# Performance work log

Measured on AMD Instinct MI355X. Metric: run time of the kernel, lower is better.

Reference implementation:

```python
import jax, jax.numpy as jnp
import numpy as np

B, S, D = 16, 2048, 2048  # S == D required for m_q + output broadcast in original code


def setup_inputs() -> dict:
    key = jax.random.key(0)
    ks = jax.random.split(key, 8)
    scale = 1.0 / np.sqrt(D)
    return {
        "hidden_list": jax.random.normal(ks[0], (B, S, D), dtype=jnp.float32),
        "m_q": jax.random.normal(ks[1], (D,), dtype=jnp.float32),
        "Wq": jax.random.normal(ks[2], (D, D), dtype=jnp.float32) * scale,
        "bq": jax.random.normal(ks[3], (D,), dtype=jnp.float32) * scale,
        "Wm": jax.random.normal(ks[4], (D, D), dtype=jnp.float32) * scale,
        "bm": jax.random.normal(ks[5], (D,), dtype=jnp.float32) * scale,
        "Wa": jax.random.normal(ks[6], (D, D), dtype=jnp.float32) * scale,
        "ba": jax.random.normal(ks[7], (D,), dtype=jnp.float32) * scale,
    }


def reference(hidden_list, m_q, Wq, bq, Wm, bm, Wa, ba):
    # hidden_list: [B, S, D]; m_q: [D]
    hq = jnp.tanh(jnp.einsum("bsd,ed->bse", hidden_list, Wq) + bq)      # [B,S,D]
    mq = jnp.tanh(Wm @ m_q + bm)                                        # [D]
    Sg = hq * mq                                                        # gated bilinear, [B,S,D]
    alpha = jax.nn.softmax(jnp.einsum("bsd,ed->bse", Sg, Wa) + ba, axis=-1)  # [B,S,D]
    output = jnp.sum(alpha * hidden_list, axis=-1)                      # [B,S]
    m_q_new = m_q + output                                              # broadcast [D]+[B,S] (S==D)
    return output, m_q_new
```

## Files before the change

### kernel.cpp

```cpp
#include <hip/hip_runtime.h>

typedef unsigned short u16;
typedef short bf16x8 __attribute__((ext_vector_type(8)));
typedef u16 u16x8 __attribute__((ext_vector_type(8)));
typedef float f32x4 __attribute__((ext_vector_type(4)));

__device__ __forceinline__ float bf2f(u16 u) {
    union { unsigned u; float f; } c; c.u = ((unsigned)u) << 16; return c.f;
}
__device__ __forceinline__ u16 f2bf(float f) {
    union { float f; unsigned u; } c; c.f = f;
    unsigned r = c.u + 0x7FFFu + ((c.u >> 16) & 1u);
    return (u16)(r >> 16);
}
__device__ __forceinline__ float tanh_fast(float x) {
    float e = __expf(2.0f * x);
    return 1.0f - 2.0f / (e + 1.0f);
}
__device__ __forceinline__ void gll16(const void* g, void* l) {
    __builtin_amdgcn_global_load_lds((const __attribute__((address_space(1))) void*)g,
                                     (__attribute__((address_space(3))) void*)l, 16, 0, 0);
}

#define BAR() __builtin_amdgcn_s_barrier()

__global__ __launch_bounds__(256) void cvt_f32_bf16(const float* __restrict__ src,
                                                    u16* __restrict__ dst, int n8) {
    int i = blockIdx.x * blockDim.x + threadIdx.x;
    int stride = gridDim.x * blockDim.x;
    for (; i < n8; i += stride) {
        const float4* s = (const float4*)(src + (size_t)i * 8);
        float4 a = s[0], b = s[1];
        u16x8 o;
        o[0] = f2bf(a.x); o[1] = f2bf(a.y); o[2] = f2bf(a.z); o[3] = f2bf(a.w);
        o[4] = f2bf(b.x); o[5] = f2bf(b.y); o[6] = f2bf(b.z); o[7] = f2bf(b.w);
        *(u16x8*)(dst + (size_t)i * 8) = o;
    }
}

__global__ __launch_bounds__(256) void mq_kernel(const float* __restrict__ Wm,
                                                 const float* __restrict__ q,
                                                 const float* __restrict__ bm,
                                                 float* __restrict__ mq, int D) {
    int w = threadIdx.x >> 6, l = threadIdx.x & 63;
    int e = blockIdx.x * 4 + w;
    const float* wp = Wm + (size_t)e * D;
    float s = 0.f;
    for (int j = 0; j < D; j += 256) {
        float4 wv = *(const float4*)(wp + j + l * 4);
        float4 qv = *(const float4*)(q + j + l * 4);
        s += wv.x * qv.x + wv.y * qv.y + wv.z * qv.z + wv.w * qv.w;
    }
    #pragma unroll
    for (int o = 32; o >= 1; o >>= 1) s += __shfl_xor(s, o);
    if (l == 0) mq[e] = tanh_fast(s + bm[e]);
}

template <int EPI>
__global__ __launch_bounds__(512, 2) void gemm8(const u16* __restrict__ A,
                                                const u16* __restrict__ B,
                                                const float* __restrict__ bias,
                                                const float* __restrict__ gate,
                                                u16* __restrict__ C,
                                                int M, int N, int K) {
    __shared__ u16 sh[65536];
    char* LDS = (char*)sh;
    const int K2 = K * 2;
    const int KT = K >> 6;

    const int tid = threadIdx.x;
    const int w = tid >> 6, l = tid & 63;
    const int wm = w >> 2, wn = w & 3;

    int orig = blockIdx.x + gridDim.x * blockIdx.y;
    int nwg = gridDim.x * gridDim.y;
    int id = ((nwg & 7) == 0) ? ((orig & 7) * (nwg >> 3) + (orig >> 3)) : orig;
    const int tileN = (id % gridDim.x) * 256;
    const int tileM = (id / gridDim.x) * 256;

    const int r0 = (w * 2) * 8 + (l >> 3);
    const int r1 = (w * 2 + 1) * 8 + (l >> 3);
    const int cc = ((l & 7) ^ (l >> 3)) << 4;
    const char* srcA0 = (const char*)A + (size_t)(tileM + r0) * K2 + cc;
    const char* srcA1 = (const char*)A + (size_t)(tileM + r1) * K2 + cc;
    const char* srcB0 = (const char*)B + (size_t)(tileN + r0) * K2 + cc;
    const char* srcB1 = (const char*)B + (size_t)(tileN + r1) * K2 + cc;
    const int ldc0 = (w * 2) * 1024, ldc1 = (w * 2 + 1) * 1024;

#define STG_A(tk, h) do { size_t go = (size_t)(tk) * 128 + (size_t)(h) * 128 * K2; \
    int sb = ((((tk) & 1) * 2 + (h)) * 16384); \
    gll16(srcA0 + go, LDS + sb + ldc0); gll16(srcA1 + go, LDS + sb + ldc1); } while (0)
#define STG_B(tk, h) do { size_t go = (size_t)(tk) * 128 + (size_t)(h) * 128 * K2; \
    int sb = 65536 + ((((tk) & 1) * 2 + (h)) * 16384); \
    gll16(srcB0 + go, LDS + sb + ldc0); gll16(srcB1 + go, LDS + sb + ldc1); } while (0)

    const int sw = l & 7;
    const int rowA = (wm * 64 + (l & 15)) * 128;
    const int rowB = (wn * 32 + (l & 15)) * 128;
    const int ck0 = (((l >> 4) ^ sw) << 4);
    const int ck1 = (((4 + (l >> 4)) ^ sw) << 4);
    const char* pA0 = LDS + rowA + ck0;
    const char* pA1 = LDS + rowA + ck1;
    const char* pB0 = LDS + 65536 + rowB + ck0;
    const char* pB1 = LDS + 65536 + rowB + ck1;

    f32x4 acc[2][4][2][2] = {};

    STG_A(0, 0); STG_B(0, 0); STG_A(0, 1); STG_B(0, 1);
    STG_A(1, 0); STG_B(1, 0);
    asm volatile("s_waitcnt vmcnt(4)" ::: "memory");
    BAR();

#define MFMA_CLUSTER(QM, QN, AF, BF)                                            \
    __builtin_amdgcn_s_setprio(1);                                              \
    _Pragma("unroll")                                                           \
    for (int fm = 0; fm < 4; ++fm)                                              \
        _Pragma("unroll")                                                       \
        for (int fn = 0; fn < 2; ++fn) {                                        \
            acc[QM][fm][QN][fn] = __builtin_amdgcn_mfma_f32_16x16x32_bf16(      \
                AF[fm][0], BF[fn][0], acc[QM][fm][QN][fn], 0, 0, 0);            \
            acc[QM][fm][QN][fn] = __builtin_amdgcn_mfma_f32_16x16x32_bf16(      \
                AF[fm][1], BF[fn][1], acc[QM][fm][QN][fn], 0, 0, 0);            \
        }                                                                       \
    __builtin_amdgcn_s_setprio(0);

#define ITER(t, P) do {                                                         \
    constexpr int A0O = (2 * (P)) * 16384;                                      \
    constexpr int A1O = (2 * (P) + 1) * 16384;                                  \
    bf16x8 af[4][2], b0[2][2], b1[2][2];                                        \
                                   \
    _Pragma("unroll")                                                           \
    for (int fm = 0; fm < 4; ++fm) {                                            \
        af[fm][0] = *(const bf16x8*)(pA0 + A0O + fm * 2048);                    \
        af[fm][1] = *(const bf16x8*)(pA1 + A0O + fm * 2048);                    \
    }                                                                           \
    _Pragma("unroll")                                                           \
    for (int fn = 0; fn < 2; ++fn) {                                            \
        b0[fn][0] = *(const bf16x8*)(pB0 + A0O + fn * 2048);                    \
        b0[fn][1] = *(const bf16x8*)(pB1 + A0O + fn * 2048);                    \
    }                                                                           \
    if ((t) + 1 < KT) STG_A((t) + 1, 1);                                        \
    BAR();                                                                      \
    MFMA_CLUSTER(0, 0, af, b0)                                                  \
    BAR();                                                                      \
                                       \
    _Pragma("unroll")                                                           \
    for (int fn = 0; fn < 2; ++fn) {                                            \
        b1[fn][0] = *(const bf16x8*)(pB0 + A1O + fn * 2048);                    \
        b1[fn][1] = *(const bf16x8*)(pB1 + A1O + fn * 2048);                    \
    }                                                                           \
    if ((t) + 1 < KT) STG_B((t) + 1, 1);                                        \
    BAR();                                                                      \
    MFMA_CLUSTER(0, 1, af, b1)                                                  \
    BAR();                                                                      \
                                       \
    _Pragma("unroll")                                                           \
    for (int fm = 0; fm < 4; ++fm) {                                            \
        af[fm][0] = *(const bf16x8*)(pA0 + A1O + fm * 2048);                    \
        af[fm][1] = *(const bf16x8*)(pA1 + A1O + fm * 2048);                    \
    }                                                                           \
    if ((t) + 2 < KT) STG_A((t) + 2, 0);                                        \
    BAR();                                                                      \
    MFMA_CLUSTER(1, 0, af, b0)                                                  \
    BAR();                                                                      \
                                     \
    if ((t) + 2 < KT) STG_B((t) + 2, 0);                                        \
    BAR();                                                                      \
    MFMA_CLUSTER(1, 1, af, b1)                                                  \
    if ((t) + 2 < KT) asm volatile("s_waitcnt vmcnt(4)" ::: "memory");          \
    else              asm volatile("s_waitcnt vmcnt(0)" ::: "memory");          \
    BAR();                                                                      \
} while (0)

    for (int tt = 0; tt < KT; tt += 2) {
        ITER(tt, 0);
        ITER(tt + 1, 1);
    }
#undef ITER
#undef MFMA_CLUSTER
#undef STG_A
#undef STG_B

    const int cr = (l >> 4) * 4;
    const int cl = l & 15;
    #pragma unroll
    for (int qn = 0; qn < 2; ++qn)
        #pragma unroll
        for (int fn = 0; fn < 2; ++fn) {
            const int col = tileN + qn * 128 + wn * 32 + fn * 16 + cl;
            const float bs = bias[col];
            float gt = 0.f;
            if (EPI == 0) gt = gate[col];
            #pragma unroll
            for (int qm = 0; qm < 2; ++qm)
                #pragma unroll
                for (int fm = 0; fm < 4; ++fm)
                    #pragma unroll
                    for (int r = 0; r < 4; ++r) {
                        const int row = tileM + qm * 128 + wm * 64 + fm * 16 + cr + r;
                        float v = acc[qm][fm][qn][fn][r] + bs;
                        if (EPI == 0) v = tanh_fast(v) * gt;
                        C[(size_t)row * N + col] = f2bf(v);
                    }
        }
}

__global__ __launch_bounds__(256) void softmax_out(const u16* __restrict__ logits,
                                                   const float* __restrict__ hidden,
                                                   const float* __restrict__ m_q,
                                                   float* __restrict__ out,
                                                   int D, int R) {
    const int r = blockIdx.x;
    const int t = threadIdx.x;
    const int w = t >> 6, l = t & 63;
    const u16* lp = logits + (size_t)r * D + t * 8;
    const float* hp = hidden + (size_t)r * D + t * 8;

    bf16x8 lv = *(const bf16x8*)lp;
    float lf[8];
    #pragma unroll
    for (int j = 0; j < 8; ++j) lf[j] = bf2f((u16)lv[j]);
    float4 h0 = *(const float4*)hp;
    float4 h1 = *(const float4*)(hp + 4);
    float hv[8] = {h0.x, h0.y, h0.z, h0.w, h1.x, h1.y, h1.z, h1.w};

    float m = lf[0];
    #pragma unroll
    for (int j = 1; j < 8; ++j) m = fmaxf(m, lf[j]);
    #pragma unroll
    for (int o = 32; o >= 1; o >>= 1) m = fmaxf(m, __shfl_xor(m, o));

    __shared__ float red[8];
    if (l == 0) red[w] = m;
    __syncthreads();
    m = fmaxf(fmaxf(red[0], red[1]), fmaxf(red[2], red[3]));
    __syncthreads();

    float se = 0.f, sh = 0.f;
    #pragma unroll
    for (int j = 0; j < 8; ++j) {
        float e = __expf(lf[j] - m);
        se += e;
        sh += e * hv[j];
    }
    #pragma unroll
    for (int o = 32; o >= 1; o >>= 1) { se += __shfl_xor(se, o); sh += __shfl_xor(sh, o); }
    if (l == 0) { red[w] = se; red[4 + w] = sh; }
    __syncthreads();
    if (t == 0) {
        float SE = red[0] + red[1] + red[2] + red[3];
        float SH = red[4] + red[5] + red[6] + red[7];
        float o = SH / SE;
        out[r] = o;
        out[R + r] = m_q[r & (D - 1)] + o;
    }
}

extern "C" void kernel_launch(void* const* d_in, const int* in_sizes, int n_in,
                              void* d_out, int out_size, void* d_ws, size_t ws_size,
                              hipStream_t stream) {
    const float* hidden = (const float*)d_in[0];
    const float* m_q    = (const float*)d_in[1];
    const float* Wq     = (const float*)d_in[2];
    const float* bq     = (const float*)d_in[3];
    const float* Wm     = (const float*)d_in[4];
    const float* bm     = (const float*)d_in[5];
    const float* Wa     = (const float*)d_in[6];
    const float* ba     = (const float*)d_in[7];
    float* out = (float*)d_out;

    const int D = 2048;
    const int M = 16 * 2048;

    char* ws = (char*)d_ws;
    size_t oH  = 0;
    size_t oS  = oH  + (size_t)M * D * 2;
    size_t oWq = oS  + (size_t)M * D * 2;
    size_t oWa = oWq + (size_t)D * D * 2;
    size_t oMq = oWa + (size_t)D * D * 2;
    size_t need = oMq + (size_t)D * sizeof(float);
    if (ws_size < need) return;

    u16* hbf    = (u16*)(ws + oH);
    u16* Sg     = (u16*)(ws + oS);
    u16* Wqb    = (u16*)(ws + oWq);
    u16* Wab    = (u16*)(ws + oWa);
    float* mq   = (float*)(ws + oMq);
    u16* logits = hbf;

    cvt_f32_bf16<<<4096, 256, 0, stream>>>(hidden, hbf, M * D / 8);
    cvt_f32_bf16<<<1024, 256, 0, stream>>>(Wq, Wqb, D * D / 8);
    cvt_f32_bf16<<<1024, 256, 0, stream>>>(Wa, Wab, D * D / 8);
    mq_kernel<<<D / 4, 256, 0, stream>>>(Wm, m_q, bm, mq, D);

    dim3 grid(D / 256, M / 256);
    gemm8<0><<<grid, 512, 0, stream>>>(hbf, Wqb, bq, mq, Sg, M, D, D);
    gemm8<1><<<grid, 512, 0, stream>>>(Sg, Wab, ba, nullptr, logits, M, D, D);

    softmax_out<<<M, 256, 0, stream>>>(logits, hidden, m_q, out, D, M);
}
```

Measured before the change: 660.4 us.

## Fuse second GEMM with online softmax and weighted row reduction

Replaces the second GEMM plus the separate softmax kernel with one kernel. Each block owns 128 rows and loops over all 8 column tiles of Wa, keeping a running max, denominator and numerator per row, so the bf16 logits matrix is never written or read back. The weighting now uses the bf16 copy of hidden instead of the fp32 original, and the block walks N sequentially, giving a 256-block grid with smaller tiles. It also adds several barriers per column tile for the cross-wave reductions.

```diff
diff --git a/kernel.cpp b/kernel.cpp
--- a/kernel.cpp
+++ b/kernel.cpp
@@ -56,7 +56,6 @@
     if (l == 0) mq[e] = tanh_fast(s + bm[e]);
 }
 
-template <int EPI>
 __global__ __launch_bounds__(512, 2) void gemm8(const u16* __restrict__ A,
                                                 const u16* __restrict__ B,
                                                 const float* __restrict__ bias,
@@ -128,7 +127,6 @@
     constexpr int A0O = (2 * (P)) * 16384;                                      \
     constexpr int A1O = (2 * (P) + 1) * 16384;                                  \
     bf16x8 af[4][2], b0[2][2], b1[2][2];                                        \
-                                   \
     _Pragma("unroll")                                                           \
     for (int fm = 0; fm < 4; ++fm) {                                            \
         af[fm][0] = *(const bf16x8*)(pA0 + A0O + fm * 2048);                    \
@@ -143,7 +141,6 @@
     BAR();                                                                      \
     MFMA_CLUSTER(0, 0, af, b0)                                                  \
     BAR();                                                                      \
-                                       \
     _Pragma("unroll")                                                           \
     for (int fn = 0; fn < 2; ++fn) {                                            \
         b1[fn][0] = *(const bf16x8*)(pB0 + A1O + fn * 2048);                    \
@@ -153,7 +150,6 @@
     BAR();                                                                      \
     MFMA_CLUSTER(0, 1, af, b1)                                                  \
     BAR();                                                                      \
-                                       \
     _Pragma("unroll")                                                           \
     for (int fm = 0; fm < 4; ++fm) {                                            \
         af[fm][0] = *(const bf16x8*)(pA0 + A1O + fm * 2048);                    \
@@ -163,7 +159,6 @@
     BAR();                                                                      \
     MFMA_CLUSTER(1, 0, af, b0)                                                  \
     BAR();                                                                      \
-                                     \
     if ((t) + 2 < KT) STG_B((t) + 2, 0);                                        \
     BAR();                                                                      \
     MFMA_CLUSTER(1, 1, af, b1)                                                  \
@@ -189,8 +184,7 @@
         for (int fn = 0; fn < 2; ++fn) {
             const int col = tileN + qn * 128 + wn * 32 + fn * 16 + cl;
             const float bs = bias[col];
-            float gt = 0.f;
-            if (EPI == 0) gt = gate[col];
+            const float gt = gate[col];
             #pragma unroll
             for (int qm = 0; qm < 2; ++qm)
                 #pragma unroll
@@ -198,61 +192,205 @@
                     #pragma unroll
                     for (int r = 0; r < 4; ++r) {
                         const int row = tileM + qm * 128 + wm * 64 + fm * 16 + cr + r;
-                        float v = acc[qm][fm][qn][fn][r] + bs;
-                        if (EPI == 0) v = tanh_fast(v) * gt;
+                        float v = tanh_fast(acc[qm][fm][qn][fn][r] + bs) * gt;
                         C[(size_t)row * N + col] = f2bf(v);
                     }
         }
 }
 
-__global__ __launch_bounds__(256) void softmax_out(const u16* __restrict__ logits,
-                                                   const float* __restrict__ hidden,
-                                                   const float* __restrict__ m_q,
-                                                   float* __restrict__ out,
-                                                   int D, int R) {
-    const int r = blockIdx.x;
-    const int t = threadIdx.x;
-    const int w = t >> 6, l = t & 63;
-    const u16* lp = logits + (size_t)r * D + t * 8;
-    const float* hp = hidden + (size_t)r * D + t * 8;
-
-    bf16x8 lv = *(const bf16x8*)lp;
-    float lf[8];
-    #pragma unroll
-    for (int j = 0; j < 8; ++j) lf[j] = bf2f((u16)lv[j]);
-    float4 h0 = *(const float4*)hp;
-    float4 h1 = *(const float4*)(hp + 4);
-    float hv[8] = {h0.x, h0.y, h0.z, h0.w, h1.x, h1.y, h1.z, h1.w};
-
-    float m = lf[0];
-    #pragma unroll
-    for (int j = 1; j < 8; ++j) m = fmaxf(m, lf[j]);
-    #pragma unroll
-    for (int o = 32; o >= 1; o >>= 1) m = fmaxf(m, __shfl_xor(m, o));
-
-    __shared__ float red[8];
-    if (l == 0) red[w] = m;
-    __syncthreads();
-    m = fmaxf(fmaxf(red[0], red[1]), fmaxf(red[2], red[3]));
-    __syncthreads();
-
-    float se = 0.f, sh = 0.f;
-    #pragma unroll
-    for (int j = 0; j < 8; ++j) {
-        float e = __expf(lf[j] - m);
-        se += e;
-        sh += e * hv[j];
+__global__ __launch_bounds__(512, 2) void gemm_sm(const u16* __restrict__ A,
+                                                  const u16* __restrict__ B,
+                                                  const float* __restrict__ bias,
+                                                  const u16* __restrict__ H,
+                                                  const float* __restrict__ m_q,
+                                                  float* __restrict__ out,
+                                                  int M, int N, int K) {
+    __shared__ u16 sh[53248];
+    char* LDS = (char*)sh;
+    const int K2 = K * 2;
+    const int KT = K >> 6;
+    const int tid = threadIdx.x;
+    const int w = tid >> 6, l = tid & 63;
+    const int wm = w >> 2, wn = w & 3;
+
+    int orig = blockIdx.x;
+    int nwg = gridDim.x;
+    int id = ((nwg & 7) == 0) ? ((orig & 7) * (nwg >> 3) + (orig >> 3)) : orig;
+    const int r0g = id * 128;
+
+    float* redmax = (float*)(LDS + 98304);
+    float* redd   = (float*)(LDS + 98304 + 2048);
+    float* redn   = (float*)(LDS + 98304 + 4096);
+    float* m_s    = (float*)(LDS + 98304 + 6144);
+    float* d_s    = (float*)(LDS + 98304 + 6656);
+    float* n_s    = (float*)(LDS + 98304 + 7168);
+    float* mrow   = (float*)(LDS + 98304 + 7680);
+
+    const int ra = l >> 3;
+    const int cc = ((l & 7) ^ ra) << 4;
+    const char* sA = (const char*)A + (size_t)(r0g + w * 16 + ra) * K2 + cc;
+    const char* sBb = (const char*)B + (size_t)(w * 32 + ra) * K2 + cc;
+    char* dA = LDS + w * 2048;
+    char* dB = LDS + 32768 + w * 4096;
+
+    const int sw = l & 7;
+    const int ck0 = (((l >> 4) ^ sw) << 4);
+    const int ck1 = (((4 + (l >> 4)) ^ sw) << 4);
+    const char* pA0 = LDS + (wm * 64 + (l & 15)) * 128 + ck0;
+    const char* pA1 = LDS + (wm * 64 + (l & 15)) * 128 + ck1;
+    const char* pB0 = LDS + 32768 + (wn * 64 + (l & 15)) * 128 + ck0;
+    const char* pB1 = LDS + 32768 + (wn * 64 + (l & 15)) * 128 + ck1;
+
+    const int cr = (l >> 4) * 4;
+    const int cl = l & 15;
+
+    if (tid < 128) { m_s[tid] = -1e30f; d_s[tid] = 0.f; n_s[tid] = 0.f; }
+    BAR();
+
+    for (int nt = 0; nt < 8; ++nt) {
+        const int n0 = nt * 256;
+        const char* sB = sBb + (size_t)n0 * K2;
+
+#define STG(tk, SLA, SLB) do { size_t go = (size_t)(tk) * 128;                  \
+    gll16(sA + go, dA + (SLA)); gll16(sA + go + (size_t)8 * K2, dA + (SLA) + 1024); \
+    gll16(sB + go, dB + (SLB)); gll16(sB + go + (size_t)8 * K2, dB + (SLB) + 1024); \
+    gll16(sB + go + (size_t)16 * K2, dB + (SLB) + 2048);                        \
+    gll16(sB + go + (size_t)24 * K2, dB + (SLB) + 3072); } while (0)
+
+        f32x4 acc[4][4] = {};
+
+        STG(0, 0, 0); STG(1, 16384, 32768);
+        asm volatile("s_waitcnt vmcnt(6)" ::: "memory");
+        BAR();
+
+#define IT(t, P) do {                                                           \
+    constexpr int SA = (P) * 16384;                                             \
+    constexpr int SB = (P) * 32768;                                             \
+    bf16x8 af[4][2], bf[4][2];                                                  \
+    _Pragma("unroll")                                                           \
+    for (int fm = 0; fm < 4; ++fm) {                                            \
+        af[fm][0] = *(const bf16x8*)(pA0 + SA + fm * 2048);                     \
+        af[fm][1] = *(const bf16x8*)(pA1 + SA + fm * 2048);                     \
+    }                                                                           \
+    _Pragma("unroll")                                                           \
+    for (int fn = 0; fn < 4; ++fn) {                                            \
+        bf[fn][0] = *(const bf16x8*)(pB0 + SB + fn * 2048);                     \
+        bf[fn][1] = *(const bf16x8*)(pB1 + SB + fn * 2048);                     \
+    }                                                                           \
+    asm volatile("s_waitcnt lgkmcnt(0)" ::: "memory");                          \
+    BAR();                                                                      \
+    if ((t) + 2 < KT) STG((t) + 2, SA, SB);                                     \
+    __builtin_amdgcn_s_setprio(1);                                              \
+    _Pragma("unroll")                                                           \
+    for (int fm = 0; fm < 4; ++fm)                                              \
+        _Pragma("unroll")                                                       \
+        for (int fn = 0; fn < 4; ++fn) {                                        \
+            acc[fm][fn] = __builtin_amdgcn_mfma_f32_16x16x32_bf16(              \
+                af[fm][0], bf[fn][0], acc[fm][fn], 0, 0, 0);                    \
+            acc[fm][fn] = __builtin_amdgcn_mfma_f32_16x16x32_bf16(              \
+                af[fm][1], bf[fn][1], acc[fm][fn], 0, 0, 0);                    \
+        }                                                                       \
+    __builtin_amdgcn_s_setprio(0);                                              \
+    if ((t) + 2 < KT)      asm volatile("s_waitcnt vmcnt(6)" ::: "memory");     \
+    else if ((t) + 1 < KT) asm volatile("s_waitcnt vmcnt(0)" ::: "memory");     \
+    BAR();                                                                      \
+} while (0)
+
+        for (int tt = 0; tt < KT; tt += 2) {
+            IT(tt, 0);
+            IT(tt + 1, 1);
+        }
+#undef IT
+#undef STG
+
+        float bs[4];
+        #pragma unroll
+        for (int fn = 0; fn < 4; ++fn) bs[fn] = bias[n0 + wn * 64 + fn * 16 + cl];
+
+        float tmax[4][4];
+        #pragma unroll
+        for (int fm = 0; fm < 4; ++fm)
+            #pragma unroll
+            for (int rr = 0; rr < 4; ++rr) {
+                float v = acc[fm][0][rr] + bs[0];
+                #pragma unroll
+                for (int fn = 1; fn < 4; ++fn) v = fmaxf(v, acc[fm][fn][rr] + bs[fn]);
+                tmax[fm][rr] = v;
+            }
+        #pragma unroll
+        for (int o = 8; o >= 1; o >>= 1)
+            #pragma unroll
+            for (int fm = 0; fm < 4; ++fm)
+                #pragma unroll
+                for (int rr = 0; rr < 4; ++rr)
+                    tmax[fm][rr] = fmaxf(tmax[fm][rr], __shfl_xor(tmax[fm][rr], o));
+        if (cl == 0) {
+            #pragma unroll
+            for (int fm = 0; fm < 4; ++fm)
+                #pragma unroll
+                for (int rr = 0; rr < 4; ++rr)
+                    redmax[(wm * 64 + fm * 16 + cr + rr) * 4 + wn] = tmax[fm][rr];
+        }
+        BAR();
+        if (tid < 128) {
+            float mt = fmaxf(fmaxf(redmax[tid * 4], redmax[tid * 4 + 1]),
+                             fmaxf(redmax[tid * 4 + 2], redmax[tid * 4 + 3]));
+            float mo = m_s[tid];
+            float mn = fmaxf(mo, mt);
+            float sc = __expf(mo - mn);
+            d_s[tid] *= sc; n_s[tid] *= sc; m_s[tid] = mn; mrow[tid] = mn;
+        }
+        BAR();
+
+        float dsum[4][4], nsum[4][4];
+        #pragma unroll
+        for (int fm = 0; fm < 4; ++fm)
+            #pragma unroll
+            for (int rr = 0; rr < 4; ++rr) {
+                const int rl = wm * 64 + fm * 16 + cr + rr;
+                const float mm = mrow[rl];
+                const u16* hp = H + (size_t)(r0g + rl) * N + n0 + wn * 64 + cl;
+                float ds = 0.f, ns = 0.f;
+                #pragma unroll
+                for (int fn = 0; fn < 4; ++fn) {
+                    float e = __expf(acc[fm][fn][rr] + bs[fn] - mm);
+                    ds += e;
+                    ns += e * bf2f(hp[fn * 16]);
+                }
+                dsum[fm][rr] = ds; nsum[fm][rr] = ns;
+            }
+        #pragma unroll
+        for (int o = 8; o >= 1; o >>= 1)
+            #pragma unroll
+            for (int fm = 0; fm < 4; ++fm)
+                #pragma unroll
+                for (int rr = 0; rr < 4; ++rr) {
+                    dsum[fm][rr] += __shfl_xor(dsum[fm][rr], o);
+                    nsum[fm][rr] += __shfl_xor(nsum[fm][rr], o);
+                }
+        if (cl == 0) {
+            #pragma unroll
+            for (int fm = 0; fm < 4; ++fm)
+                #pragma unroll
+                for (int rr = 0; rr < 4; ++rr) {
+                    const int rl = wm * 64 + fm * 16 + cr + rr;
+                    redd[rl * 4 + wn] = dsum[fm][rr];
+                    redn[rl * 4 + wn] = nsum[fm][rr];
+                }
+        }
+        BAR();
+        if (tid < 128) {
+            d_s[tid] += redd[tid * 4] + redd[tid * 4 + 1] + redd[tid * 4 + 2] + redd[tid * 4 + 3];
+            n_s[tid] += redn[tid * 4] + redn[tid * 4 + 1] + redn[tid * 4 + 2] + redn[tid * 4 + 3];
+        }
+        BAR();
     }
-    #pragma unroll
-    for (int o = 32; o >= 1; o >>= 1) { se += __shfl_xor(se, o); sh += __shfl_xor(sh, o); }
-    if (l == 0) { red[w] = se; red[4 + w] = sh; }
-    __syncthreads();
-    if (t == 0) {
-        float SE = red[0] + red[1] + red[2] + red[3];
-        float SH = red[4] + red[5] + red[6] + red[7];
-        float o = SH / SE;
-        out[r] = o;
-        out[R + r] = m_q[r & (D - 1)] + o;
+
+    if (tid < 128) {
+        const int rg = r0g + tid;
+        float o = n_s[tid] / d_s[tid];
+        out[rg] = o;
+        out[M + rg] = m_q[rg & (N - 1)] + o;
     }
 }
 
@@ -286,7 +424,6 @@
     u16* Wqb    = (u16*)(ws + oWq);
     u16* Wab    = (u16*)(ws + oWa);
     float* mq   = (float*)(ws + oMq);
-    u16* logits = hbf;
 
     cvt_f32_bf16<<<4096, 256, 0, stream>>>(hidden, hbf, M * D / 8);
     cvt_f32_bf16<<<1024, 256, 0, stream>>>(Wq, Wqb, D * D / 8);
@@ -294,8 +431,7 @@
     mq_kernel<<<D / 4, 256, 0, stream>>>(Wm, m_q, bm, mq, D);
 
     dim3 grid(D / 256, M / 256);
-    gemm8<0><<<grid, 512, 0, stream>>>(hbf, Wqb, bq, mq, Sg, M, D, D);
-    gemm8<1><<<grid, 512, 0, stream>>>(Sg, Wab, ba, nullptr, logits, M, D, D);
-
-    softmax_out<<<M, 256, 0, stream>>>(logits, hidden, m_q, out, D, M);
-}
+    gemm8<<<grid, 512, 0, stream>>>(hbf, Wqb, bq, mq, Sg, M, D, D);
+
+    gemm_sm<<<M / 128, 512, 0, stream>>>(Sg, Wab, ba, hbf, m_q, out, M, D, D);
+}
```

New measurement: 717.6 us. 1.09x slower.

## Fuse softmax-weighted reduction into second GEMM epilogue with split-N partials

Applied to the files above, without the earlier changes.

The second GEMM now computes per-tile row max, exp-sum and hidden-weighted exp-sum in its epilogue and writes three small partial arrays per 256-column tile, instead of writing the full bf16 logits matrix. A tiny pass2 kernel merges the eight partials per row with a log-sum-exp rescale to produce the output. This removes the logits write and the separate softmax kernel's re-read of logits and fp32 hidden. In exchange the epilogue adds LDS reductions, extra barriers and strided bf16 reads of hidden, and uses bf16 hidden values instead of fp32 in the weighted sum.

```diff
diff --git a/kernel.cpp b/kernel.cpp
--- a/kernel.cpp
+++ b/kernel.cpp
@@ -56,36 +56,36 @@
     if (l == 0) mq[e] = tanh_fast(s + bm[e]);
 }
 
-template <int EPI>
-__global__ __launch_bounds__(512, 2) void gemm8(const u16* __restrict__ A,
-                                                const u16* __restrict__ B,
-                                                const float* __restrict__ bias,
-                                                const float* __restrict__ gate,
-                                                u16* __restrict__ C,
-                                                int M, int N, int K) {
-    __shared__ u16 sh[65536];
-    char* LDS = (char*)sh;
-    const int K2 = K * 2;
-    const int KT = K >> 6;
-
-    const int tid = threadIdx.x;
-    const int w = tid >> 6, l = tid & 63;
-    const int wm = w >> 2, wn = w & 3;
-
-    int orig = blockIdx.x + gridDim.x * blockIdx.y;
-    int nwg = gridDim.x * gridDim.y;
-    int id = ((nwg & 7) == 0) ? ((orig & 7) * (nwg >> 3) + (orig >> 3)) : orig;
-    const int tileN = (id % gridDim.x) * 256;
-    const int tileM = (id / gridDim.x) * 256;
-
-    const int r0 = (w * 2) * 8 + (l >> 3);
-    const int r1 = (w * 2 + 1) * 8 + (l >> 3);
-    const int cc = ((l & 7) ^ (l >> 3)) << 4;
-    const char* srcA0 = (const char*)A + (size_t)(tileM + r0) * K2 + cc;
-    const char* srcA1 = (const char*)A + (size_t)(tileM + r1) * K2 + cc;
-    const char* srcB0 = (const char*)B + (size_t)(tileN + r0) * K2 + cc;
-    const char* srcB1 = (const char*)B + (size_t)(tileN + r1) * K2 + cc;
-    const int ldc0 = (w * 2) * 1024, ldc1 = (w * 2 + 1) * 1024;
+#define GEMM_PREAMBLE()                                                          \
+    __shared__ u16 sh[65536];                                                    \
+    char* LDS = (char*)sh;                                                       \
+    const int K2 = K * 2;                                                        \
+    const int KT = K >> 6;                                                       \
+    const int tid = threadIdx.x;                                                 \
+    const int w = tid >> 6, l = tid & 63;                                        \
+    const int wm = w >> 2, wn = w & 3;                                           \
+    int orig = blockIdx.x + gridDim.x * blockIdx.y;                              \
+    int nwg = gridDim.x * gridDim.y;                                             \
+    int id = ((nwg & 7) == 0) ? ((orig & 7) * (nwg >> 3) + (orig >> 3)) : orig;  \
+    const int tileN = (id % gridDim.x) * 256;                                    \
+    const int tileM = (id / gridDim.x) * 256;                                    \
+    const int r0 = (w * 2) * 8 + (l >> 3);                                       \
+    const int r1 = (w * 2 + 1) * 8 + (l >> 3);                                   \
+    const int cc = ((l & 7) ^ (l >> 3)) << 4;                                    \
+    const char* srcA0 = (const char*)A + (size_t)(tileM + r0) * K2 + cc;         \
+    const char* srcA1 = (const char*)A + (size_t)(tileM + r1) * K2 + cc;         \
+    const char* srcB0 = (const char*)B + (size_t)(tileN + r0) * K2 + cc;         \
+    const char* srcB1 = (const char*)B + (size_t)(tileN + r1) * K2 + cc;         \
+    const int ldc0 = (w * 2) * 1024, ldc1 = (w * 2 + 1) * 1024;                  \
+    const int sw = l & 7;                                                        \
+    const int rowA = (wm * 64 + (l & 15)) * 128;                                 \
+    const int rowB = (wn * 32 + (l & 15)) * 128;                                 \
+    const int ck0 = (((l >> 4) ^ sw) << 4);                                      \
+    const int ck1 = (((4 + (l >> 4)) ^ sw) << 4);                                \
+    const char* pA0 = LDS + rowA + ck0;                                          \
+    const char* pA1 = LDS + rowA + ck1;                                          \
+    const char* pB0 = LDS + 65536 + rowB + ck0;                                  \
+    const char* pB1 = LDS + 65536 + rowB + ck1;
 
 #define STG_A(tk, h) do { size_t go = (size_t)(tk) * 128 + (size_t)(h) * 128 * K2; \
     int sb = ((((tk) & 1) * 2 + (h)) * 16384); \
@@ -93,23 +93,6 @@
 #define STG_B(tk, h) do { size_t go = (size_t)(tk) * 128 + (size_t)(h) * 128 * K2; \
     int sb = 65536 + ((((tk) & 1) * 2 + (h)) * 16384); \
     gll16(srcB0 + go, LDS + sb + ldc0); gll16(srcB1 + go, LDS + sb + ldc1); } while (0)
-
-    const int sw = l & 7;
-    const int rowA = (wm * 64 + (l & 15)) * 128;
-    const int rowB = (wn * 32 + (l & 15)) * 128;
-    const int ck0 = (((l >> 4) ^ sw) << 4);
-    const int ck1 = (((4 + (l >> 4)) ^ sw) << 4);
-    const char* pA0 = LDS + rowA + ck0;
-    const char* pA1 = LDS + rowA + ck1;
-    const char* pB0 = LDS + 65536 + rowB + ck0;
-    const char* pB1 = LDS + 65536 + rowB + ck1;
-
-    f32x4 acc[2][4][2][2] = {};
-
-    STG_A(0, 0); STG_B(0, 0); STG_A(0, 1); STG_B(0, 1);
-    STG_A(1, 0); STG_B(1, 0);
-    asm volatile("s_waitcnt vmcnt(4)" ::: "memory");
-    BAR();
 
 #define MFMA_CLUSTER(QM, QN, AF, BF)                                            \
     __builtin_amdgcn_s_setprio(1);                                              \
@@ -128,7 +111,6 @@
     constexpr int A0O = (2 * (P)) * 16384;                                      \
     constexpr int A1O = (2 * (P) + 1) * 16384;                                  \
     bf16x8 af[4][2], b0[2][2], b1[2][2];                                        \
-                                   \
     _Pragma("unroll")                                                           \
     for (int fm = 0; fm < 4; ++fm) {                                            \
         af[fm][0] = *(const bf16x8*)(pA0 + A0O + fm * 2048);                    \
@@ -143,7 +125,6 @@
     BAR();                                                                      \
     MFMA_CLUSTER(0, 0, af, b0)                                                  \
     BAR();                                                                      \
-                                       \
     _Pragma("unroll")                                                           \
     for (int fn = 0; fn < 2; ++fn) {                                            \
         b1[fn][0] = *(const bf16x8*)(pB0 + A1O + fn * 2048);                    \
@@ -153,7 +134,6 @@
     BAR();                                                                      \
     MFMA_CLUSTER(0, 1, af, b1)                                                  \
     BAR();                                                                      \
-                                       \
     _Pragma("unroll")                                                           \
     for (int fm = 0; fm < 4; ++fm) {                                            \
         af[fm][0] = *(const bf16x8*)(pA0 + A1O + fm * 2048);                    \
@@ -163,7 +143,6 @@
     BAR();                                                                      \
     MFMA_CLUSTER(1, 0, af, b0)                                                  \
     BAR();                                                                      \
-                                     \
     if ((t) + 2 < KT) STG_B((t) + 2, 0);                                        \
     BAR();                                                                      \
     MFMA_CLUSTER(1, 1, af, b1)                                                  \
@@ -172,14 +151,25 @@
     BAR();                                                                      \
 } while (0)
 
-    for (int tt = 0; tt < KT; tt += 2) {
-        ITER(tt, 0);
-        ITER(tt + 1, 1);
-    }
-#undef ITER
-#undef MFMA_CLUSTER
-#undef STG_A
-#undef STG_B
+#define GEMM_KLOOP()                                                            \
+    STG_A(0, 0); STG_B(0, 0); STG_A(0, 1); STG_B(0, 1);                         \
+    STG_A(1, 0); STG_B(1, 0);                                                   \
+    asm volatile("s_waitcnt vmcnt(4)" ::: "memory");                            \
+    BAR();                                                                      \
+    for (int tt = 0; tt < KT; tt += 2) {                                        \
+        ITER(tt, 0);                                                            \
+        ITER(tt + 1, 1);                                                        \
+    }
+
+__global__ __launch_bounds__(512, 2) void gemm8(const u16* __restrict__ A,
+                                                const u16* __restrict__ B,
+                                                const float* __restrict__ bias,
+                                                const float* __restrict__ gate,
+                                                u16* __restrict__ C,
+                                                int M, int N, int K) {
+    GEMM_PREAMBLE()
+    f32x4 acc[2][4][2][2] = {};
+    GEMM_KLOOP()
 
     const int cr = (l >> 4) * 4;
     const int cl = l & 15;
@@ -189,8 +179,7 @@
         for (int fn = 0; fn < 2; ++fn) {
             const int col = tileN + qn * 128 + wn * 32 + fn * 16 + cl;
             const float bs = bias[col];
-            float gt = 0.f;
-            if (EPI == 0) gt = gate[col];
+            const float gt = gate[col];
             #pragma unroll
             for (int qm = 0; qm < 2; ++qm)
                 #pragma unroll
@@ -198,62 +187,131 @@
                     #pragma unroll
                     for (int r = 0; r < 4; ++r) {
                         const int row = tileM + qm * 128 + wm * 64 + fm * 16 + cr + r;
-                        float v = acc[qm][fm][qn][fn][r] + bs;
-                        if (EPI == 0) v = tanh_fast(v) * gt;
+                        float v = tanh_fast(acc[qm][fm][qn][fn][r] + bs) * gt;
                         C[(size_t)row * N + col] = f2bf(v);
                     }
         }
 }
 
-__global__ __launch_bounds__(256) void softmax_out(const u16* __restrict__ logits,
-                                                   const float* __restrict__ hidden,
-                                                   const float* __restrict__ m_q,
-                                                   float* __restrict__ out,
-                                                   int D, int R) {
-    const int r = blockIdx.x;
-    const int t = threadIdx.x;
-    const int w = t >> 6, l = t & 63;
-    const u16* lp = logits + (size_t)r * D + t * 8;
-    const float* hp = hidden + (size_t)r * D + t * 8;
-
-    bf16x8 lv = *(const bf16x8*)lp;
-    float lf[8];
-    #pragma unroll
-    for (int j = 0; j < 8; ++j) lf[j] = bf2f((u16)lv[j]);
-    float4 h0 = *(const float4*)hp;
-    float4 h1 = *(const float4*)(hp + 4);
-    float hv[8] = {h0.x, h0.y, h0.z, h0.w, h1.x, h1.y, h1.z, h1.w};
-
-    float m = lf[0];
-    #pragma unroll
-    for (int j = 1; j < 8; ++j) m = fmaxf(m, lf[j]);
-    #pragma unroll
-    for (int o = 32; o >= 1; o >>= 1) m = fmaxf(m, __shfl_xor(m, o));
-
-    __shared__ float red[8];
-    if (l == 0) red[w] = m;
-    __syncthreads();
-    m = fmaxf(fmaxf(red[0], red[1]), fmaxf(red[2], red[3]));
-    __syncthreads();
-
-    float se = 0.f, sh = 0.f;
+__global__ __launch_bounds__(512, 2) void gemm2p(const u16* __restrict__ A,
+                                                 const u16* __restrict__ B,
+                                                 const float* __restrict__ bias,
+                                                 const u16* __restrict__ H,
+                                                 float* __restrict__ pmax,
+                                                 float* __restrict__ pden,
+                                                 float* __restrict__ pnum,
+                                                 int M, int N, int K) {
+    GEMM_PREAMBLE()
+    f32x4 acc[2][4][2][2] = {};
+    GEMM_KLOOP()
+
+    const int cr = (l >> 4) * 4;
+    const int cl = l & 15;
+    const int NT = N >> 8;
+    float* redA = (float*)LDS;
+    float* redD = (float*)(LDS + 4096);
+    float* redN = (float*)(LDS + 8192);
+    float* rowmax = (float*)(LDS + 12288);
+
+    float bs[2][2];
+    #pragma unroll
+    for (int qn = 0; qn < 2; ++qn)
+        #pragma unroll
+        for (int fn = 0; fn < 2; ++fn)
+            bs[qn][fn] = bias[tileN + qn * 128 + wn * 32 + fn * 16 + cl];
+
+    #pragma unroll
+    for (int qm = 0; qm < 2; ++qm)
+        #pragma unroll
+        for (int fm = 0; fm < 4; ++fm)
+            #pragma unroll
+            for (int rr = 0; rr < 4; ++rr) {
+                float v = -1e30f;
+                #pragma unroll
+                for (int qn = 0; qn < 2; ++qn)
+                    #pragma unroll
+                    for (int fn = 0; fn < 2; ++fn)
+                        v = fmaxf(v, acc[qm][fm][qn][fn][rr] + bs[qn][fn]);
+                #pragma unroll
+                for (int o = 8; o >= 1; o >>= 1) v = fmaxf(v, __shfl_xor(v, o));
+                if (cl == 0)
+                    redA[(qm * 128 + wm * 64 + fm * 16 + cr + rr) * 4 + wn] = v;
+            }
+    BAR();
+    if (tid < 256)
+        rowmax[tid] = fmaxf(fmaxf(redA[tid * 4], redA[tid * 4 + 1]),
+                            fmaxf(redA[tid * 4 + 2], redA[tid * 4 + 3]));
+    BAR();
+
+    const u16* hbase = H + tileN + wn * 32 + cl;
+    #pragma unroll
+    for (int qm = 0; qm < 2; ++qm)
+        #pragma unroll
+        for (int fm = 0; fm < 4; ++fm)
+            #pragma unroll
+            for (int rr = 0; rr < 4; ++rr) {
+                const int rl = qm * 128 + wm * 64 + fm * 16 + cr + rr;
+                const float mm = rowmax[rl];
+                const u16* hp = hbase + (size_t)(tileM + rl) * N;
+                float ds = 0.f, ns = 0.f;
+                #pragma unroll
+                for (int qn = 0; qn < 2; ++qn)
+                    #pragma unroll
+                    for (int fn = 0; fn < 2; ++fn) {
+                        float e = __expf(acc[qm][fm][qn][fn][rr] + bs[qn][fn] - mm);
+                        ds += e;
+                        ns += e * bf2f(hp[qn * 128 + fn * 16]);
+                    }
+                #pragma unroll
+                for (int o = 8; o >= 1; o >>= 1) {
+                    ds += __shfl_xor(ds, o);
+                    ns += __shfl_xor(ns, o);
+                }
+                if (cl == 0) {
+                    redD[rl * 4 + wn] = ds;
+                    redN[rl * 4 + wn] = ns;
+                }
+            }
+    BAR();
+    if (tid < 256) {
+        float d = redD[tid * 4] + redD[tid * 4 + 1] + redD[tid * 4 + 2] + redD[tid * 4 + 3];
+        float n = redN[tid * 4] + redN[tid * 4 + 1] + redN[tid * 4 + 2] + redN[tid * 4 + 3];
+        const size_t idx = (size_t)(tileM + tid) * NT + (tileN >> 8);
+        pmax[idx] = rowmax[tid];
+        pden[idx] = d;
+        pnum[idx] = n;
+    }
+}
+
+__global__ __launch_bounds__(256) void pass2(const float* __restrict__ pmax,
+                                             const float* __restrict__ pden,
+                                             const float* __restrict__ pnum,
+                                             const float* __restrict__ m_q,
+                                             float* __restrict__ out,
+                                             int M, int D) {
+    int rg = blockIdx.x * 256 + threadIdx.x;
+    const float4* pm = (const float4*)(pmax + (size_t)rg * 8);
+    const float4* pd = (const float4*)(pden + (size_t)rg * 8);
+    const float4* pn = (const float4*)(pnum + (size_t)rg * 8);
+    float4 m0 = pm[0], m1 = pm[1];
+    float4 d0 = pd[0], d1 = pd[1];
+    float4 n0 = pn[0], n1 = pn[1];
+    float mv[8] = {m0.x, m0.y, m0.z, m0.w, m1.x, m1.y, m1.z, m1.w};
+    float dv[8] = {d0.x, d0.y, d0.z, d0.w, d1.x, d1.y, d1.z, d1.w};
+    float nv[8] = {n0.x, n0.y, n0.z, n0.w, n1.x, n1.y, n1.z, n1.w};
+    float mg = mv[0];
+    #pragma unroll
+    for (int j = 1; j < 8; ++j) mg = fmaxf(mg, mv[j]);
+    float den = 0.f, num = 0.f;
     #pragma unroll
     for (int j = 0; j < 8; ++j) {
-        float e = __expf(lf[j] - m);
-        se += e;
-        sh += e * hv[j];
-    }
-    #pragma unroll
-    for (int o = 32; o >= 1; o >>= 1) { se += __shfl_xor(se, o); sh += __shfl_xor(sh, o); }
-    if (l == 0) { red[w] = se; red[4 + w] = sh; }
-    __syncthreads();
-    if (t == 0) {
-        float SE = red[0] + red[1] + red[2] + red[3];
-        float SH = red[4] + red[5] + red[6] + red[7];
-        float o = SH / SE;
-        out[r] = o;
-        out[R + r] = m_q[r & (D - 1)] + o;
-    }
+        float e = __expf(mv[j] - mg);
+        den += dv[j] * e;
+        num += nv[j] * e;
+    }
+    float o = num / den;
+    out[rg] = o;
+    out[M + rg] = m_q[rg & (D - 1)] + o;
 }
 
 extern "C" void kernel_launch(void* const* d_in, const int* in_sizes, int n_in,
@@ -278,7 +336,10 @@
     size_t oWq = oS  + (size_t)M * D * 2;
     size_t oWa = oWq + (size_t)D * D * 2;
     size_t oMq = oWa + (size_t)D * D * 2;
-    size_t need = oMq + (size_t)D * sizeof(float);
+    size_t oPM = oMq + (size_t)D * sizeof(float);
+    size_t oPD = oPM + (size_t)M * 8 * sizeof(float);
+    size_t oPN = oPD + (size_t)M * 8 * sizeof(float);
+    size_t need = oPN + (size_t)M * 8 * sizeof(float);
     if (ws_size < need) return;
 
     u16* hbf    = (u16*)(ws + oH);
@@ -286,7 +347,9 @@
     u16* Wqb    = (u16*)(ws + oWq);
     u16* Wab    = (u16*)(ws + oWa);
     float* mq   = (float*)(ws + oMq);
-    u16* logits = hbf;
+    float* pM   = (float*)(ws + oPM);
+    float* pD   = (float*)(ws + oPD);
+    float* pN   = (float*)(ws + oPN);
 
     cvt_f32_bf16<<<4096, 256, 0, stream>>>(hidden, hbf, M * D / 8);
     cvt_f32_bf16<<<1024, 256, 0, stream>>>(Wq, Wqb, D * D / 8);
@@ -294,8 +357,8 @@
     mq_kernel<<<D / 4, 256, 0, stream>>>(Wm, m_q, bm, mq, D);
 
     dim3 grid(D / 256, M / 256);
-    gemm8<0><<<grid, 512, 0, stream>>>(hbf, Wqb, bq, mq, Sg, M, D, D);
-    gemm8<1><<<grid, 512, 0, stream>>>(Sg, Wab, ba, nullptr, logits, M, D, D);
-
-    softmax_out<<<M, 256, 0, stream>>>(logits, hidden, m_q, out, D, M);
-}
+    gemm8<<<grid, 512, 0, stream>>>(hbf, Wqb, bq, mq, Sg, M, D, D);
+    gemm2p<<<grid, 512, 0, stream>>>(Sg, Wab, ba, hbf, pM, pD, pN, M, D, D);
+
+    pass2<<<M / 256, 256, 0, stream>>>(pM, pD, pN, m_q, out, M, D);
+}
```

Result: no change. 659.3 us (-0.2%).
